# Kernel optimization log

Hardware: AMD Instinct MI355X
Metric: run time of the kernel (lower is better)

## Reference

```python
import jax, jax.numpy as jnp
import numpy as np

K = 3        # kernel_size
STRIDE = 1
PAD = 1
DIL = 1


def setup_inputs() -> dict:
    key = jax.random.key(0)
    k1, k2, k3 = jax.random.split(key, 3)
    B, C, H, W = 8, 256, 64, 64
    O = 256
    x = jax.random.normal(k1, (B, C, H, W), jnp.float32)
    # offset conv: Conv2d(C, 2*K*K, K, stride, pad) with bias
    w_off = jax.random.normal(k2, (2 * K * K, C, K, K), jnp.float32) * 0.01
    b_off = jnp.zeros((2 * K * K,), jnp.float32)
    # DeformConv weight (mmcv DeformConv has no bias)
    w_dcn = jax.random.normal(k3, (O, C, K, K), jnp.float32) * (1.0 / np.sqrt(C * K * K))
    return {"x": x, "w_off": w_off, "b_off": b_off, "w_dcn": w_dcn}


def _conv(x, w):
    return jax.lax.conv_general_dilated(
        x, w, window_strides=(STRIDE, STRIDE),
        padding=[(PAD, PAD), (PAD, PAD)], rhs_dilation=(DIL, DIL),
        dimension_numbers=("NCHW", "OIHW", "NCHW"))


def _bilinear(img_flat, y, x, H, W):
    # img_flat: [C, H*W]; y, x: [KK, Ho, Wo] float sampling coords
    y0 = jnp.floor(y)
    x0 = jnp.floor(x)
    out = jnp.zeros((img_flat.shape[0],) + y.shape, img_flat.dtype)
    for dy in (0.0, 1.0):
        for dx in (0.0, 1.0):
            yi = y0 + dy
            xi = x0 + dx
            wgt = (1.0 - jnp.abs(y - yi)) * (1.0 - jnp.abs(x - xi))
            valid = (yi >= 0) & (yi < H) & (xi >= 0) & (xi < W)
            yc = jnp.clip(yi, 0, H - 1).astype(jnp.int32)
            xc = jnp.clip(xi, 0, W - 1).astype(jnp.int32)
            idx = yc * W + xc                       # [KK,Ho,Wo]
            g = jnp.take(img_flat, idx.reshape(-1), axis=1)
            g = g.reshape((img_flat.shape[0],) + y.shape)  # [C,KK,Ho,Wo]
            out = out + g * (wgt * valid)[None]
    return out


def reference(x, w_off, b_off, w_dcn):
    B, C, H, W = x.shape
    O = w_dcn.shape[0]
    # 1) predict offsets: [B, 2*K*K, Ho, Wo], channel order (ky,kx) pairs per tap
    offset = _conv(x, w_off) + b_off[None, :, None, None]
    Ho, Wo = offset.shape[2], offset.shape[3]
    off = offset.reshape(B, K * K, 2, Ho, Wo)
    off_y = off[:, :, 0]   # [B,KK,Ho,Wo]
    off_x = off[:, :, 1]
    # 2) base sampling grid for a standard conv
    ky, kx = jnp.meshgrid(jnp.arange(K), jnp.arange(K), indexing="ij")
    ky = ky.reshape(-1).astype(x.dtype)   # [KK]
    kx = kx.reshape(-1).astype(x.dtype)
    hy = (jnp.arange(Ho) * STRIDE - PAD).astype(x.dtype)
    wx = (jnp.arange(Wo) * STRIDE - PAD).astype(x.dtype)
    base_y = hy[None, :, None] + (ky * DIL)[:, None, None]  # [KK,Ho,1]
    base_x = wx[None, None, :] + (kx * DIL)[:, None, None]  # [KK,1,Wo]
    sy = off_y + base_y[None]   # [B,KK,Ho,Wo]
    sx = off_x + base_x[None]
    # 3) bilinear gather: sampled patches [B,C,KK,Ho,Wo]
    img_flat = x.reshape(B, C, H * W)
    sampled = jax.vmap(lambda im, yy, xx: _bilinear(im, yy, xx, H, W))(img_flat, sy, sx)
    # 4) weighted sum over (C, kernel taps)
    out = jnp.einsum("bckhw,ock->bohw", sampled, w_dcn.reshape(O, C, K * K))
    return out
```

## Files before the change

### kernel.cpp

```cpp
#include <hip/hip_runtime.h>
#include <hip/hip_bf16.h>


#define HW 64
#define CCH 256
#define OCH 256
#define BB 8
#define KDIM 2304

typedef __attribute__((ext_vector_type(8))) short bf16x8;
typedef __attribute__((ext_vector_type(8))) unsigned short u16x8;
typedef __attribute__((ext_vector_type(4))) float f32x4;
typedef __attribute__((ext_vector_type(2))) float f32x2;
typedef __attribute__((ext_vector_type(4))) unsigned short u16x4;
typedef __attribute__((ext_vector_type(4))) unsigned int u32x4;

static __device__ inline unsigned short f2bf(float f) {
  unsigned u = __builtin_bit_cast(unsigned, f);
  u += 0x7FFFu + ((u >> 16) & 1u);
  return (unsigned short)(u >> 16);
}
static __device__ inline float bf2f(unsigned short s) {
  return __builtin_bit_cast(float, (unsigned)s << 16);
}
static __device__ inline unsigned cvt_pk_bf16(float lo, float hi) {
  unsigned r;
  asm("v_cvt_pk_bf16_f32 %0, %1, %2" : "=v"(r) : "v"(lo), "v"(hi));
  return r;
}

#define GLL16(gsrc, ldst)                                                      \
  __builtin_amdgcn_global_load_lds(                                           \
      (const __attribute__((address_space(1))) void*)(gsrc),                  \
      (__attribute__((address_space(3))) void*)(ldst), 16, 0, 0)

static __device__ inline int xcd_swz256(int bid) {
  return (bid & 7) * 32 + (bid >> 3);
}

__global__ __launch_bounds__(256) void prep(const float* __restrict__ w_dcn,
                                            const float* __restrict__ w_off,
                                            unsigned short* __restrict__ W2,
                                            unsigned short* __restrict__ Wop,
                                            unsigned short* __restrict__ zp) {
  int i = blockIdx.x * 256 + threadIdx.x;
  if (i < 9 * 256 * 256) {
    int o = i / KDIM;
    int r = i - o * KDIM;
    int kk = r >> 8, c = r & 255;
    W2[i] = f2bf(w_dcn[((o << 8) + c) * 9 + kk]);
  }
  if (i < 32 * KDIM) {
    int n = i / KDIM;
    int r = i - n * KDIM;
    int kk = r >> 8, c = r & 255;
    Wop[i] = (n < 18) ? f2bf(w_off[((n << 8) + c) * 9 + kk]) : (unsigned short)0;
  }
  if (i < 512) zp[i] = 0;
}

__global__ __launch_bounds__(256) void xpose(const float* __restrict__ x,
                                             unsigned short* __restrict__ xTbf) {
  __shared__ float t[64][65];
  const int tid = threadIdx.x;
  const int bid = blockIdx.x;
  const int ct = bid & 3;
  const int pt = (bid >> 2) & 63;
  const int b = bid >> 8;
#pragma unroll
  for (int i = 0; i < 16; ++i) {
    int cl = i * 4 + (tid >> 6);
    int p = tid & 63;
    t[cl][p] = x[(((b << 8) + ct * 64 + cl) << 12) + pt * 64 + p];
  }
  __syncthreads();
#pragma unroll
  for (int i = 0; i < 4; ++i) {
    int pl = i * 16 + (tid >> 4);
    int c4 = (tid & 15) * 4;
    u16x4 v;
    v[0] = f2bf(t[c4][pl]);
    v[1] = f2bf(t[c4 + 1][pl]);
    v[2] = f2bf(t[c4 + 2][pl]);
    v[3] = f2bf(t[c4 + 3][pl]);
    *(u16x4*)(xTbf + (((size_t)((b << 12) + pt * 64 + pl)) << 8) + ct * 64 + c4) = v;
  }
}

__global__ __launch_bounds__(256) void offset_gemm(
    const unsigned short* __restrict__ xTbf, const unsigned short* __restrict__ Wop,
    const unsigned short* __restrict__ zp, const float* __restrict__ b_off,
    float* __restrict__ off_buf) {
  __shared__ short ldsA[2][128 * 32];
  __shared__ short ldsB[2][32 * 32];
  const int tid = threadIdx.x;
  const int lane = tid & 63;
  const int wid = __builtin_amdgcn_readfirstlane(tid >> 6);
  const int m0 = xcd_swz256(blockIdx.x) * 128;
  const int b = m0 >> 12;
  const unsigned short* xb = xTbf + ((size_t)b << 20);

  int hA[2], wA[2], scA[2];
#pragma unroll
  for (int g = 0; g < 2; ++g) {
    int r = wid * 32 + g * 16 + (lane >> 2);
    int pos = (m0 & 4095) + r;
    hA[g] = pos >> 6;
    wA[g] = pos & 63;
    scA[g] = ((lane & 3) ^ ((r >> 1) & 3)) * 8;
  }
  const int rB = wid * 16 + (lane >> 2);
  const unsigned short* srcB =
      Wop + (size_t)rB * KDIM + ((lane & 3) ^ ((rB >> 1) & 3)) * 8;

  const int l15 = lane & 15, l4 = lane >> 4;
  int offA[2], offB[2];
#pragma unroll
  for (int f = 0; f < 2; ++f) {
    int rA = wid * 32 + f * 16 + l15;
    offA[f] = rA * 32 + ((l4 ^ ((rA >> 1) & 3)) << 3);
    int rb = f * 16 + l15;
    offB[f] = rb * 32 + ((l4 ^ ((rb >> 1) & 3)) << 3);
  }

  const f32x4 z = {0.f, 0.f, 0.f, 0.f};
  f32x4 acc[2][2];
#pragma unroll
  for (int i = 0; i < 2; ++i)
#pragma unroll
    for (int j = 0; j < 2; ++j) acc[i][j] = z;

  auto stage = [&](int buf, int t) {
    const int kk = t >> 3;
    const int c0 = (t & 7) * 32;
    const int dy = kk / 3 - 1, dx = kk - (kk / 3) * 3 - 1;
#pragma unroll
    for (int g = 0; g < 2; ++g) {
      const int y = hA[g] + dy, xx = wA[g] + dx;
      const bool valid = ((unsigned)y < 64u) && ((unsigned)xx < 64u);
      const unsigned short* src =
          valid ? xb + ((((y << 6) + xx) << 8) + c0 + scA[g]) : zp + scA[g];
      GLL16(src, &ldsA[buf][((wid * 2 + g) * 64 + lane) * 8]);
    }
    if (wid < 2) GLL16(srcB + t * 32, &ldsB[buf][(wid * 64 + lane) * 8]);
  };

  stage(0, 0);
  __syncthreads();

  for (int t = 0; t < 72; ++t) {
    const int buf = t & 1;
    if (t < 71) stage(buf ^ 1, t + 1);
    bf16x8 af[2], bfr[2];
#pragma unroll
    for (int f = 0; f < 2; ++f) af[f] = *(const bf16x8*)&ldsA[buf][offA[f]];
#pragma unroll
    for (int f = 0; f < 2; ++f) bfr[f] = *(const bf16x8*)&ldsB[buf][offB[f]];
#pragma unroll
    for (int i = 0; i < 2; ++i)
#pragma unroll
      for (int j = 0; j < 2; ++j)
        acc[i][j] = __builtin_amdgcn_mfma_f32_16x16x32_bf16(af[i], bfr[j],
                                                            acc[i][j], 0, 0, 0);
    __syncthreads();
  }

#pragma unroll
  for (int j = 0; j < 2; ++j) {
    const int col = j * 16 + l15;
    if (col < 18) {
      const float bias = b_off[col];
#pragma unroll
      for (int i = 0; i < 2; ++i)
#pragma unroll
        for (int r = 0; r < 4; ++r) {
          const int m = m0 + wid * 32 + i * 16 + l4 * 4 + r;
          off_buf[(size_t)m * 18 + col] = acc[i][j][r] + bias;
        }
    }
  }
}

__global__ __launch_bounds__(512, 2) void dcn_fused(
    const unsigned short* __restrict__ xTbf, const float* __restrict__ off_buf,
    const unsigned short* __restrict__ W2, float* __restrict__ out) {
  __shared__ f32x2 slyx[128][9];
  __shared__ u16x4 spos[128][9];
  __shared__ short ldsA[2][128 * 64];
  __shared__ short ldsB[2][256 * 64];

  const int tid = threadIdx.x;
  const int lane = tid & 63;
  const int wid = __builtin_amdgcn_readfirstlane(tid >> 6);
  const int m0 = xcd_swz256(blockIdx.x) * 128;
  const int b = m0 >> 12;
  const unsigned short* xb = xTbf + ((size_t)b << 20);

  for (int idx = tid; idx < 128 * 9; idx += 512) {
    const int r = idx / 9, k = idx - (idx / 9) * 9;
    const int ky = k / 3, kx = k - ky * 3;
    const int pos = (m0 & 4095) + r;
    const int h = pos >> 6, w = pos & 63;
    const float offy = off_buf[(size_t)(m0 + r) * 18 + 2 * k];
    const float offx = off_buf[(size_t)(m0 + r) * 18 + 2 * k + 1];
    const float sy = offy + (float)(h - 1 + ky);
    const float sx = offx + (float)(w - 1 + kx);
    const float y0f = floorf(sy), x0f = floorf(sx);
    const int y0 = (int)y0f, x0 = (int)x0f;
    const int y1 = y0 + 1, x1 = x0 + 1;
    const unsigned vy0 = ((unsigned)y0 < 64u), vy1 = ((unsigned)y1 < 64u);
    const unsigned vx0 = ((unsigned)x0 < 64u), vx1 = ((unsigned)x1 < 64u);
    const int y0c = min(max(y0, 0), HW - 1), y1c = min(max(y1, 0), HW - 1);
    const int x0c = min(max(x0, 0), HW - 1), x1c = min(max(x1, 0), HW - 1);
    f32x2 lyx;
    lyx[0] = sy - y0f;
    lyx[1] = sx - x0f;
    u16x4 pp;
    pp[0] = (unsigned short)(((y0c << 6) + x0c) | ((vy0 & vx0) << 15));
    pp[1] = (unsigned short)(((y0c << 6) + x1c) | ((vy0 & vx1) << 15));
    pp[2] = (unsigned short)(((y1c << 6) + x0c) | ((vy1 & vx0) << 15));
    pp[3] = (unsigned short)(((y1c << 6) + x1c) | ((vy1 & vx1) << 15));
    slyx[r][k] = lyx;
    spos[r][k] = pp;
  }

  const int r = tid >> 2, q = tid & 3;
  const int dstA0 = r * 64 + (((2 * q) ^ (r & 7)) << 3);
  const int dstA1 = r * 64 + (((2 * q + 1) ^ (r & 7)) << 3);

  const unsigned short* srcBp[4];
  int dstB[4];
#pragma unroll
  for (int g = 0; g < 4; ++g) {
    const int idx = g * 512 + tid;
    const int row = idx >> 3, c = idx & 7;
    srcBp[g] = W2 + (size_t)row * KDIM + ((c ^ (row & 7)) << 3);
    dstB[g] = idx * 8;
  }

  const int l15 = lane & 15, l4 = lane >> 4;
  const int wm = wid & 1, wn = wid >> 1;
  int offA[4][2], offB[4][2];
#pragma unroll
  for (int f = 0; f < 4; ++f) {
    const int rA = wm * 64 + f * 16 + l15;
    const int rB = wn * 64 + f * 16 + l15;
#pragma unroll
    for (int h = 0; h < 2; ++h) {
      offA[f][h] = rA * 64 + (((h * 4 + l4) ^ (rA & 7)) << 3);
      offB[f][h] = rB * 64 + (((h * 4 + l4) ^ (rB & 7)) << 3);
    }
  }

  const f32x4 z = {0.f, 0.f, 0.f, 0.f};
  f32x4 acc[4][4];
#pragma unroll
  for (int i = 0; i < 4; ++i)
#pragma unroll
    for (int j = 0; j < 4; ++j) acc[i][j] = z;

  __syncthreads();

  f32x4 wv;
  int av[4];
  auto load_params = [&](int tap) {
    const f32x2 lyx = slyx[r][tap];
    const u16x4 pp = spos[r][tap];
    const float ly = lyx[0], lx = lyx[1];
#pragma unroll
    for (int e = 0; e < 4; ++e) av[e] = (int)(pp[e] & 0x0FFFu) << 8;
    wv[0] = (1.f - ly) * (1.f - lx) * (float)(pp[0] >> 15);
    wv[1] = (1.f - ly) * lx * (float)(pp[1] >> 15);
    wv[2] = ly * (1.f - lx) * (float)(pp[2] >> 15);
    wv[3] = ly * lx * (float)(pp[3] >> 15);
  };

  u16x8 gc0[2], gc1[2], gc2[2], gc3[2];
  f32x4 gw;

  auto issue_gathers = [&](int t) {
    const int cb = ((t & 3) << 6) + q * 16;
#pragma unroll
    for (int h = 0; h < 2; ++h) {
      gc0[h] = *(const u16x8*)(xb + av[0] + cb + h * 8);
      gc1[h] = *(const u16x8*)(xb + av[1] + cb + h * 8);
      gc2[h] = *(const u16x8*)(xb + av[2] + cb + h * 8);
      gc3[h] = *(const u16x8*)(xb + av[3] + cb + h * 8);
    }
    gw = wv;
  };

  auto lerp_store = [&](int buf) {
    short* base = ldsA[buf];
#pragma unroll
    for (int h = 0; h < 2; ++h) {
      u32x4 wds;
#pragma unroll
      for (int e = 0; e < 4; ++e) {
        const float f0 = gw[0] * bf2f(gc0[h][2 * e]) + gw[1] * bf2f(gc1[h][2 * e]) +
                         gw[2] * bf2f(gc2[h][2 * e]) + gw[3] * bf2f(gc3[h][2 * e]);
        const float f1 = gw[0] * bf2f(gc0[h][2 * e + 1]) +
                         gw[1] * bf2f(gc1[h][2 * e + 1]) +
                         gw[2] * bf2f(gc2[h][2 * e + 1]) +
                         gw[3] * bf2f(gc3[h][2 * e + 1]);
        wds[e] = cvt_pk_bf16(f0, f1);
      }
      *(u32x4*)&base[h == 0 ? dstA0 : dstA1] = wds;
    }
  };

  load_params(0);
  issue_gathers(0);
  lerp_store(0);
#pragma unroll
  for (int g = 0; g < 4; ++g) GLL16(srcBp[g], &ldsB[0][dstB[g]]);
  __syncthreads();

  for (int t = 0; t < 36; ++t) {
    const int buf = t & 1;
    if (t < 35) {
      const int tn = t + 1;
#pragma unroll
      for (int g = 0; g < 4; ++g) GLL16(srcBp[g] + tn * 64, &ldsB[buf ^ 1][dstB[g]]);
      if ((tn & 3) == 0) load_params(tn >> 2);
      issue_gathers(tn);
    }
#pragma unroll
    for (int h = 0; h < 2; ++h) {
      bf16x8 af[4], bfr[4];
#pragma unroll
      for (int f = 0; f < 4; ++f) {
        af[f] = *(const bf16x8*)&ldsA[buf][offA[f][h]];
        bfr[f] = *(const bf16x8*)&ldsB[buf][offB[f][h]];
      }
#pragma unroll
      for (int i = 0; i < 4; ++i)
#pragma unroll
        for (int j = 0; j < 4; ++j)
          acc[i][j] = __builtin_amdgcn_mfma_f32_16x16x32_bf16(af[i], bfr[j],
                                                              acc[i][j], 0, 0, 0);
    }
    if (t < 35) lerp_store(buf ^ 1);
    __syncthreads();
  }

#pragma unroll
  for (int i = 0; i < 4; ++i) {
    const int m = m0 + wm * 64 + i * 16 + l4 * 4;
    const int bb = m >> 12;
    const int pos = m & 4095;
#pragma unroll
    for (int j = 0; j < 4; ++j) {
      const int o = wn * 64 + j * 16 + l15;
      *(f32x4*)(out + (((size_t)bb * OCH + o) << 12) + pos) = acc[i][j];
    }
  }
}

extern "C" void kernel_launch(void* const* d_in, const int* in_sizes, int n_in,
                              void* d_out, int out_size, void* d_ws,
                              size_t ws_size, hipStream_t stream) {
  const float* x = (const float*)d_in[0];
  const float* w_off = (const float*)d_in[1];
  const float* b_off = (const float*)d_in[2];
  const float* w_dcn = (const float*)d_in[3];
  float* out = (float*)d_out;

  char* ws = (char*)d_ws;
  float* off_buf = (float*)(ws);
  unsigned short* Wop = (unsigned short*)(ws + 2359296);
  unsigned short* zp = (unsigned short*)(ws + 2506752);
  unsigned short* W2 = (unsigned short*)(ws + 2507776);
  unsigned short* xTbf = (unsigned short*)(ws + 3687424);

  prep<<<2304, 256, 0, stream>>>(w_dcn, w_off, W2, Wop, zp);
  xpose<<<2048, 256, 0, stream>>>(x, xTbf);
  offset_gemm<<<256, 256, 0, stream>>>(xTbf, Wop, zp, b_off, off_buf);
  dcn_fused<<<256, 512, 0, stream>>>(xTbf, off_buf, W2, out);
}
```

Baseline: 124.4 us.

## Warp-specialize fused DCN kernel into producer gather waves and MFMA consumer waves

Splits the 8 waves of the fused deformable-conv GEMM into 4 producer waves and 4 consumer waves. The producers do the bilinear gathers, the lerp into LDS and the async weight loads. The consumers only read LDS and issue MFMAs, each over a 64x128 tile, with raised priority. The K-step shrinks from 64 to 32, which halves LDS buffers and doubles the iteration count, and gathers are prefetched two steps ahead with manual waitcnt and barrier handshakes. The aim is to overlap the latency-bound gather and lerp work with tensor-core compute. The cost is more barriers, higher register pressure in consumers (128 accumulator floats), and fragile hand-written vmcnt counts.

```diff
diff --git a/kernel.cpp b/kernel.cpp
--- a/kernel.cpp
+++ b/kernel.cpp
@@ -186,8 +186,8 @@
     const unsigned short* __restrict__ W2, float* __restrict__ out) {
   __shared__ f32x2 slyx[128][9];
   __shared__ u16x4 spos[128][9];
-  __shared__ short ldsA[2][128 * 64];
-  __shared__ short ldsB[2][256 * 64];
+  __shared__ short ldsA[2][128 * 32];
+  __shared__ short ldsB[2][256 * 32];
 
   const int tid = threadIdx.x;
   const int lane = tid & 63;
@@ -223,136 +223,176 @@
     slyx[r][k] = lyx;
     spos[r][k] = pp;
   }
-
-  const int r = tid >> 2, q = tid & 3;
-  const int dstA0 = r * 64 + (((2 * q) ^ (r & 7)) << 3);
-  const int dstA1 = r * 64 + (((2 * q + 1) ^ (r & 7)) << 3);
-
-  const unsigned short* srcBp[4];
-  int dstB[4];
-#pragma unroll
-  for (int g = 0; g < 4; ++g) {
-    const int idx = g * 512 + tid;
-    const int row = idx >> 3, c = idx & 7;
-    srcBp[g] = W2 + (size_t)row * KDIM + ((c ^ (row & 7)) << 3);
-    dstB[g] = idx * 8;
-  }
-
-  const int l15 = lane & 15, l4 = lane >> 4;
-  const int wm = wid & 1, wn = wid >> 1;
-  int offA[4][2], offB[4][2];
-#pragma unroll
-  for (int f = 0; f < 4; ++f) {
-    const int rA = wm * 64 + f * 16 + l15;
-    const int rB = wn * 64 + f * 16 + l15;
-#pragma unroll
-    for (int h = 0; h < 2; ++h) {
-      offA[f][h] = rA * 64 + (((h * 4 + l4) ^ (rA & 7)) << 3);
-      offB[f][h] = rB * 64 + (((h * 4 + l4) ^ (rB & 7)) << 3);
-    }
-  }
-
-  const f32x4 z = {0.f, 0.f, 0.f, 0.f};
-  f32x4 acc[4][4];
-#pragma unroll
-  for (int i = 0; i < 4; ++i)
-#pragma unroll
-    for (int j = 0; j < 4; ++j) acc[i][j] = z;
-
   __syncthreads();
 
-  f32x4 wv;
-  int av[4];
-  auto load_params = [&](int tap) {
-    const f32x2 lyx = slyx[r][tap];
-    const u16x4 pp = spos[r][tap];
-    const float ly = lyx[0], lx = lyx[1];
-#pragma unroll
-    for (int e = 0; e < 4; ++e) av[e] = (int)(pp[e] & 0x0FFFu) << 8;
-    wv[0] = (1.f - ly) * (1.f - lx) * (float)(pp[0] >> 15);
-    wv[1] = (1.f - ly) * lx * (float)(pp[1] >> 15);
-    wv[2] = ly * (1.f - lx) * (float)(pp[2] >> 15);
-    wv[3] = ly * lx * (float)(pp[3] >> 15);
-  };
-
-  u16x8 gc0[2], gc1[2], gc2[2], gc3[2];
-  f32x4 gw;
-
-  auto issue_gathers = [&](int t) {
-    const int cb = ((t & 3) << 6) + q * 16;
-#pragma unroll
-    for (int h = 0; h < 2; ++h) {
-      gc0[h] = *(const u16x8*)(xb + av[0] + cb + h * 8);
-      gc1[h] = *(const u16x8*)(xb + av[1] + cb + h * 8);
-      gc2[h] = *(const u16x8*)(xb + av[2] + cb + h * 8);
-      gc3[h] = *(const u16x8*)(xb + av[3] + cb + h * 8);
-    }
-    gw = wv;
-  };
-
-  auto lerp_store = [&](int buf) {
-    short* base = ldsA[buf];
-#pragma unroll
-    for (int h = 0; h < 2; ++h) {
-      u32x4 wds;
-#pragma unroll
-      for (int e = 0; e < 4; ++e) {
-        const float f0 = gw[0] * bf2f(gc0[h][2 * e]) + gw[1] * bf2f(gc1[h][2 * e]) +
-                         gw[2] * bf2f(gc2[h][2 * e]) + gw[3] * bf2f(gc3[h][2 * e]);
-        const float f1 = gw[0] * bf2f(gc0[h][2 * e + 1]) +
-                         gw[1] * bf2f(gc1[h][2 * e + 1]) +
-                         gw[2] * bf2f(gc2[h][2 * e + 1]) +
-                         gw[3] * bf2f(gc3[h][2 * e + 1]);
-        wds[e] = cvt_pk_bf16(f0, f1);
+  if (wid < 4) {
+    const int ptid = tid;
+    const int r = ptid >> 1;
+    const int g2 = ptid & 1;
+    const int g2h = g2 * 16;
+    const int dstA0 = r * 32 + (((2 * g2) ^ ((r >> 1) & 3)) << 3);
+    const int dstA1 = r * 32 + (((2 * g2 + 1) ^ ((r >> 1) & 3)) << 3);
+    const unsigned short* srcBp[4];
+    int dstB[4];
+#pragma unroll
+    for (int g = 0; g < 4; ++g) {
+      const int idx = g * 256 + ptid;
+      const int row = idx >> 2, c = idx & 3;
+      srcBp[g] = W2 + (size_t)row * KDIM + ((c ^ ((row >> 1) & 3)) << 3);
+      dstB[g] = idx * 8;
+    }
+
+    f32x4 wv;
+    int av[4];
+    auto load_params = [&](int tap) {
+      const f32x2 lyx = slyx[r][tap];
+      const u16x4 pp = spos[r][tap];
+      const float ly = lyx[0], lx = lyx[1];
+#pragma unroll
+      for (int e = 0; e < 4; ++e) av[e] = (int)(pp[e] & 0x0FFFu) << 8;
+      wv[0] = (1.f - ly) * (1.f - lx) * (float)(pp[0] >> 15);
+      wv[1] = (1.f - ly) * lx * (float)(pp[1] >> 15);
+      wv[2] = ly * (1.f - lx) * (float)(pp[2] >> 15);
+      wv[3] = ly * lx * (float)(pp[3] >> 15);
+    };
+
+    auto lerp_store = [&](int buf, const u16x8 (&gc)[4][2], const f32x4& gw) {
+#pragma unroll
+      for (int h = 0; h < 2; ++h) {
+        u32x4 wds;
+#pragma unroll
+        for (int e = 0; e < 4; ++e) {
+          const float f0 =
+              gw[0] * bf2f(gc[0][h][2 * e]) + gw[1] * bf2f(gc[1][h][2 * e]) +
+              gw[2] * bf2f(gc[2][h][2 * e]) + gw[3] * bf2f(gc[3][h][2 * e]);
+          const float f1 = gw[0] * bf2f(gc[0][h][2 * e + 1]) +
+                           gw[1] * bf2f(gc[1][h][2 * e + 1]) +
+                           gw[2] * bf2f(gc[2][h][2 * e + 1]) +
+                           gw[3] * bf2f(gc[3][h][2 * e + 1]);
+          wds[e] = cvt_pk_bf16(f0, f1);
+        }
+        *(u32x4*)&ldsA[buf][h == 0 ? dstA0 : dstA1] = wds;
       }
-      *(u32x4*)&base[h == 0 ? dstA0 : dstA1] = wds;
-    }
-  };
-
-  load_params(0);
-  issue_gathers(0);
-  lerp_store(0);
-#pragma unroll
-  for (int g = 0; g < 4; ++g) GLL16(srcBp[g], &ldsB[0][dstB[g]]);
-  __syncthreads();
-
-  for (int t = 0; t < 36; ++t) {
-    const int buf = t & 1;
-    if (t < 35) {
-      const int tn = t + 1;
-#pragma unroll
-      for (int g = 0; g < 4; ++g) GLL16(srcBp[g] + tn * 64, &ldsB[buf ^ 1][dstB[g]]);
-      if ((tn & 3) == 0) load_params(tn >> 2);
-      issue_gathers(tn);
-    }
-#pragma unroll
-    for (int h = 0; h < 2; ++h) {
-      bf16x8 af[4], bfr[4];
-#pragma unroll
-      for (int f = 0; f < 4; ++f) {
-        af[f] = *(const bf16x8*)&ldsA[buf][offA[f][h]];
-        bfr[f] = *(const bf16x8*)&ldsB[buf][offB[f][h]];
+    };
+
+    u16x8 gA[4][2], gB[4][2];
+    f32x4 wA, wB;
+
+    load_params(0);
+    {
+#pragma unroll
+      for (int c = 0; c < 4; ++c) {
+        gA[c][0] = *(const u16x8*)(xb + av[c] + g2h);
+        gA[c][1] = *(const u16x8*)(xb + av[c] + g2h + 8);
       }
+      wA = wv;
+    }
+#pragma unroll
+    for (int g = 0; g < 4; ++g) GLL16(srcBp[g], &ldsB[0][dstB[g]]);
+    __builtin_amdgcn_sched_barrier(0);
+    lerp_store(0, gA, wA);
+    {
+#pragma unroll
+      for (int c = 0; c < 4; ++c) {
+        gA[c][0] = *(const u16x8*)(xb + av[c] + 32 + g2h);
+        gA[c][1] = *(const u16x8*)(xb + av[c] + 32 + g2h + 8);
+      }
+      wA = wv;
+    }
+    asm volatile("s_waitcnt vmcnt(8) lgkmcnt(0)" ::: "memory");
+    __builtin_amdgcn_s_barrier();
+
+#define PSTEP(T, IN, INW, OUT, OUTW)                                           \
+  {                                                                            \
+    const int tn = (T) + 1;                                                    \
+    _Pragma("unroll") for (int g = 0; g < 4; ++g)                              \
+        GLL16(srcBp[g] + tn * 32, &ldsB[tn & 1][dstB[g]]);                     \
+    __builtin_amdgcn_sched_barrier(0);                                         \
+    {                                                                          \
+      const int tg = (T) + 2;                                                  \
+      if ((tg & 7) == 0) load_params(tg >> 3);                                 \
+      const int cb = ((tg & 7) << 5) + g2h;                                    \
+      _Pragma("unroll") for (int c = 0; c < 4; ++c) {                          \
+        OUT[c][0] = *(const u16x8*)(xb + av[c] + cb);                          \
+        OUT[c][1] = *(const u16x8*)(xb + av[c] + cb + 8);                      \
+      }                                                                        \
+      OUTW = wv;                                                               \
+    }                                                                          \
+    lerp_store(tn & 1, IN, INW);                                               \
+    asm volatile("s_waitcnt vmcnt(8) lgkmcnt(0)" ::: "memory");                \
+    __builtin_amdgcn_s_barrier();                                              \
+  }
+
+    for (int it = 0; it < 35; ++it) {
+      const int t0 = it * 2;
+      PSTEP(t0, gA, wA, gB, wB)
+      PSTEP(t0 + 1, gB, wB, gA, wA)
+    }
+#undef PSTEP
+    {
+#pragma unroll
+      for (int g = 0; g < 4; ++g) GLL16(srcBp[g] + 71 * 32, &ldsB[1][dstB[g]]);
+      __builtin_amdgcn_sched_barrier(0);
+      lerp_store(1, gA, wA);
+      asm volatile("s_waitcnt vmcnt(0) lgkmcnt(0)" ::: "memory");
+      __builtin_amdgcn_s_barrier();
+    }
+  } else {
+    const int wc = wid - 4;
+    const int wm = wc & 1, wn = wc >> 1;
+    const int l15 = lane & 15, l4 = lane >> 4;
+    int offA[4], offB[8];
+#pragma unroll
+    for (int f = 0; f < 4; ++f) {
+      const int rA = wm * 64 + f * 16 + l15;
+      offA[f] = rA * 32 + ((l4 ^ ((rA >> 1) & 3)) << 3);
+    }
+#pragma unroll
+    for (int j = 0; j < 8; ++j) {
+      const int rB = wn * 128 + j * 16 + l15;
+      offB[j] = rB * 32 + ((l4 ^ ((rB >> 1) & 3)) << 3);
+    }
+
+    const f32x4 z = {0.f, 0.f, 0.f, 0.f};
+    f32x4 acc[4][8];
+#pragma unroll
+    for (int i = 0; i < 4; ++i)
+#pragma unroll
+      for (int j = 0; j < 8; ++j) acc[i][j] = z;
+
+    __builtin_amdgcn_s_barrier();
+
+    for (int t = 0; t < 72; ++t) {
+      const int buf = t & 1;
+      bf16x8 af[4], bfr[8];
+#pragma unroll
+      for (int f = 0; f < 4; ++f) af[f] = *(const bf16x8*)&ldsA[buf][offA[f]];
+#pragma unroll
+      for (int j = 0; j < 8; ++j) bfr[j] = *(const bf16x8*)&ldsB[buf][offB[j]];
+      __builtin_amdgcn_s_setprio(1);
 #pragma unroll
       for (int i = 0; i < 4; ++i)
 #pragma unroll
-        for (int j = 0; j < 4; ++j)
+        for (int j = 0; j < 8; ++j)
           acc[i][j] = __builtin_amdgcn_mfma_f32_16x16x32_bf16(af[i], bfr[j],
                                                               acc[i][j], 0, 0, 0);
-    }
-    if (t < 35) lerp_store(buf ^ 1);
-    __syncthreads();
-  }
-
-#pragma unroll
-  for (int i = 0; i < 4; ++i) {
-    const int m = m0 + wm * 64 + i * 16 + l4 * 4;
-    const int bb = m >> 12;
-    const int pos = m & 4095;
-#pragma unroll
-    for (int j = 0; j < 4; ++j) {
-      const int o = wn * 64 + j * 16 + l15;
-      *(f32x4*)(out + (((size_t)bb * OCH + o) << 12) + pos) = acc[i][j];
+      __builtin_amdgcn_s_setprio(0);
+      if (t < 71) {
+        asm volatile("s_waitcnt lgkmcnt(0)" ::: "memory");
+        __builtin_amdgcn_s_barrier();
+      }
+    }
+
+#pragma unroll
+    for (int i = 0; i < 4; ++i) {
+      const int m = m0 + wm * 64 + i * 16 + l4 * 4;
+      const int bb = m >> 12;
+      const int pos = m & 4095;
+#pragma unroll
+      for (int j = 0; j < 8; ++j) {
+        const int o = wn * 128 + j * 16 + l15;
+        *(f32x4*)(out + (((size_t)bb * OCH + o) << 12) + pos) = acc[i][j];
+      }
     }
   }
 }
```

After: 128.0 us. 1.03x slower.

## Stage spatial window of input in LDS per channel chunk for deformable gather

Applied to the files above, without the earlier changes.

Changes the bf16 transposed input layout to channel-chunked blocks of 32 channels. The DCN kernel loops channel chunk outer and tap inner. For each chunk it stages a 12-row spatial window of the input into LDS, and the bilinear gathers read from it when the sample falls inside the window, otherwise from global memory. The K-step shrinks to 32, and the MFMA issue gets raised priority. The goal is to replace scattered global gathers with LDS reads. The cost is more barriers, a stall whenever the window is reloaded, and more LDS use, which may lower occupancy.

```diff
diff --git a/kernel.cpp b/kernel.cpp
--- a/kernel.cpp
+++ b/kernel.cpp
@@ -78,12 +78,15 @@
   for (int i = 0; i < 4; ++i) {
     int pl = i * 16 + (tid >> 4);
     int c4 = (tid & 15) * 4;
+    int c = ct * 64 + c4;
+    int pos = pt * 64 + pl;
     u16x4 v;
     v[0] = f2bf(t[c4][pl]);
     v[1] = f2bf(t[c4 + 1][pl]);
     v[2] = f2bf(t[c4 + 2][pl]);
     v[3] = f2bf(t[c4 + 3][pl]);
-    *(u16x4*)(xTbf + (((size_t)((b << 12) + pt * 64 + pl)) << 8) + ct * 64 + c4) = v;
+    *(u16x4*)(xTbf + ((size_t)b << 20) + (c >> 5) * 131072 + pos * 32 +
+              (c & 31)) = v;
   }
 }
 
@@ -132,14 +135,15 @@
 
   auto stage = [&](int buf, int t) {
     const int kk = t >> 3;
-    const int c0 = (t & 7) * 32;
+    const int cc = t & 7;
     const int dy = kk / 3 - 1, dx = kk - (kk / 3) * 3 - 1;
 #pragma unroll
     for (int g = 0; g < 2; ++g) {
       const int y = hA[g] + dy, xx = wA[g] + dx;
       const bool valid = ((unsigned)y < 64u) && ((unsigned)xx < 64u);
       const unsigned short* src =
-          valid ? xb + ((((y << 6) + xx) << 8) + c0 + scA[g]) : zp + scA[g];
+          valid ? xb + cc * 131072 + ((y << 6) + xx) * 32 + scA[g]
+                : zp + scA[g];
       GLL16(src, &ldsA[buf][((wid * 2 + g) * 64 + lane) * 8]);
     }
     if (wid < 2) GLL16(srcB + t * 32, &ldsB[buf][(wid * 64 + lane) * 8]);
@@ -186,8 +190,9 @@
     const unsigned short* __restrict__ W2, float* __restrict__ out) {
   __shared__ f32x2 slyx[128][9];
   __shared__ u16x4 spos[128][9];
-  __shared__ short ldsA[2][128 * 64];
-  __shared__ short ldsB[2][256 * 64];
+  __shared__ short win[12 * 64 * 32];
+  __shared__ short ldsA[2][128 * 32];
+  __shared__ short ldsB[2][256 * 32];
 
   const int tid = threadIdx.x;
   const int lane = tid & 63;
@@ -195,7 +200,23 @@
   const int m0 = xcd_swz256(blockIdx.x) * 128;
   const int b = m0 >> 12;
   const unsigned short* xb = xTbf + ((size_t)b << 20);
-
+  const int h0 = (m0 & 4095) >> 6;
+  const int ys = max(0, h0 - 5);
+
+  auto stage_window = [&](int cc) {
+    const unsigned short* xbc = xb + cc * 131072;
+#pragma unroll
+    for (int g = 0; g < 6; ++g) {
+      const int o = g * 8192 + tid * 16;
+      const int rel = o >> 12;
+      const int xw = (o >> 6) & 63;
+      const int cs = (o & 63) >> 1;
+      const int ysrc = min(63, ys + rel);
+      GLL16(xbc + ((ysrc << 6) + xw) * 32 + cs, &win[o >> 1]);
+    }
+  };
+
+  stage_window(0);
   for (int idx = tid; idx < 128 * 9; idx += 512) {
     const int r = idx / 9, k = idx - (idx / 9) * 9;
     const int ky = k / 3, kx = k - ky * 3;
@@ -212,11 +233,13 @@
     const unsigned vx0 = ((unsigned)x0 < 64u), vx1 = ((unsigned)x1 < 64u);
     const int y0c = min(max(y0, 0), HW - 1), y1c = min(max(y1, 0), HW - 1);
     const int x0c = min(max(x0, 0), HW - 1), x1c = min(max(x1, 0), HW - 1);
+    const unsigned inwin = (y0c >= ys) & (y1c <= ys + 11);
     f32x2 lyx;
     lyx[0] = sy - y0f;
     lyx[1] = sx - x0f;
     u16x4 pp;
-    pp[0] = (unsigned short)(((y0c << 6) + x0c) | ((vy0 & vx0) << 15));
+    pp[0] = (unsigned short)(((y0c << 6) + x0c) | (inwin << 14) |
+                             ((vy0 & vx0) << 15));
     pp[1] = (unsigned short)(((y0c << 6) + x1c) | ((vy0 & vx1) << 15));
     pp[2] = (unsigned short)(((y1c << 6) + x0c) | ((vy1 & vx0) << 15));
     pp[3] = (unsigned short)(((y1c << 6) + x1c) | ((vy1 & vx1) << 15));
@@ -225,31 +248,27 @@
   }
 
   const int r = tid >> 2, q = tid & 3;
-  const int dstA0 = r * 64 + (((2 * q) ^ (r & 7)) << 3);
-  const int dstA1 = r * 64 + (((2 * q + 1) ^ (r & 7)) << 3);
-
-  const unsigned short* srcBp[4];
-  int dstB[4];
-#pragma unroll
-  for (int g = 0; g < 4; ++g) {
+  const int q8 = q * 8;
+  const int dstA = r * 32 + ((q ^ ((r >> 1) & 3)) << 3);
+  const unsigned short* srcBp[2];
+  int dstB[2];
+#pragma unroll
+  for (int g = 0; g < 2; ++g) {
     const int idx = g * 512 + tid;
-    const int row = idx >> 3, c = idx & 7;
-    srcBp[g] = W2 + (size_t)row * KDIM + ((c ^ (row & 7)) << 3);
+    const int row = idx >> 2, c = idx & 3;
+    srcBp[g] = W2 + (size_t)row * KDIM + ((c ^ ((row >> 1) & 3)) << 3);
     dstB[g] = idx * 8;
   }
 
   const int l15 = lane & 15, l4 = lane >> 4;
   const int wm = wid & 1, wn = wid >> 1;
-  int offA[4][2], offB[4][2];
+  int offA[4], offB[4];
 #pragma unroll
   for (int f = 0; f < 4; ++f) {
     const int rA = wm * 64 + f * 16 + l15;
+    offA[f] = rA * 32 + ((l4 ^ ((rA >> 1) & 3)) << 3);
     const int rB = wn * 64 + f * 16 + l15;
-#pragma unroll
-    for (int h = 0; h < 2; ++h) {
-      offA[f][h] = rA * 64 + (((h * 4 + l4) ^ (rA & 7)) << 3);
-      offB[f][h] = rB * 64 + (((h * 4 + l4) ^ (rB & 7)) << 3);
-    }
+    offB[f] = rB * 32 + ((l4 ^ ((rB >> 1) & 3)) << 3);
   }
 
   const f32x4 z = {0.f, 0.f, 0.f, 0.f};
@@ -259,89 +278,85 @@
 #pragma unroll
     for (int j = 0; j < 4; ++j) acc[i][j] = z;
 
-  __syncthreads();
-
-  f32x4 wv;
-  int av[4];
-  auto load_params = [&](int tap) {
+  auto produce = [&](int buf, int tap, int cc) {
     const f32x2 lyx = slyx[r][tap];
     const u16x4 pp = spos[r][tap];
     const float ly = lyx[0], lx = lyx[1];
-#pragma unroll
-    for (int e = 0; e < 4; ++e) av[e] = (int)(pp[e] & 0x0FFFu) << 8;
-    wv[0] = (1.f - ly) * (1.f - lx) * (float)(pp[0] >> 15);
-    wv[1] = (1.f - ly) * lx * (float)(pp[1] >> 15);
-    wv[2] = ly * (1.f - lx) * (float)(pp[2] >> 15);
-    wv[3] = ly * lx * (float)(pp[3] >> 15);
+    const float w0 = (1.f - ly) * (1.f - lx) * (float)(pp[0] >> 15);
+    const float w1 = (1.f - ly) * lx * (float)(pp[1] >> 15);
+    const float w2 = ly * (1.f - lx) * (float)(pp[2] >> 15);
+    const float w3 = ly * lx * (float)(pp[3] >> 15);
+    int po[4];
+#pragma unroll
+    for (int e = 0; e < 4; ++e) po[e] = pp[e] & 0x0FFF;
+    u16x8 c[4];
+    if (__builtin_expect((pp[0] >> 14) & 1, 1)) {
+#pragma unroll
+      for (int e = 0; e < 4; ++e)
+        c[e] = *(const u16x8*)&win[((po[e] >> 6) - ys) * 2048 +
+                                   (po[e] & 63) * 32 + q8];
+    } else {
+      const unsigned short* xbc = xb + cc * 131072;
+#pragma unroll
+      for (int e = 0; e < 4; ++e)
+        c[e] = *(const u16x8*)(xbc + po[e] * 32 + q8);
+    }
+    u32x4 wds;
+#pragma unroll
+    for (int e = 0; e < 4; ++e) {
+      const float f0 = w0 * bf2f(c[0][2 * e]) + w1 * bf2f(c[1][2 * e]) +
+                       w2 * bf2f(c[2][2 * e]) + w3 * bf2f(c[3][2 * e]);
+      const float f1 = w0 * bf2f(c[0][2 * e + 1]) + w1 * bf2f(c[1][2 * e + 1]) +
+                       w2 * bf2f(c[2][2 * e + 1]) + w3 * bf2f(c[3][2 * e + 1]);
+      wds[e] = cvt_pk_bf16(f0, f1);
+    }
+    *(u32x4*)&ldsA[buf][dstA] = wds;
   };
 
-  u16x8 gc0[2], gc1[2], gc2[2], gc3[2];
-  f32x4 gw;
-
-  auto issue_gathers = [&](int t) {
-    const int cb = ((t & 3) << 6) + q * 16;
-#pragma unroll
-    for (int h = 0; h < 2; ++h) {
-      gc0[h] = *(const u16x8*)(xb + av[0] + cb + h * 8);
-      gc1[h] = *(const u16x8*)(xb + av[1] + cb + h * 8);
-      gc2[h] = *(const u16x8*)(xb + av[2] + cb + h * 8);
-      gc3[h] = *(const u16x8*)(xb + av[3] + cb + h * 8);
-    }
-    gw = wv;
-  };
-
-  auto lerp_store = [&](int buf) {
-    short* base = ldsA[buf];
-#pragma unroll
-    for (int h = 0; h < 2; ++h) {
-      u32x4 wds;
-#pragma unroll
-      for (int e = 0; e < 4; ++e) {
-        const float f0 = gw[0] * bf2f(gc0[h][2 * e]) + gw[1] * bf2f(gc1[h][2 * e]) +
-                         gw[2] * bf2f(gc2[h][2 * e]) + gw[3] * bf2f(gc3[h][2 * e]);
-        const float f1 = gw[0] * bf2f(gc0[h][2 * e + 1]) +
-                         gw[1] * bf2f(gc1[h][2 * e + 1]) +
-                         gw[2] * bf2f(gc2[h][2 * e + 1]) +
-                         gw[3] * bf2f(gc3[h][2 * e + 1]);
-        wds[e] = cvt_pk_bf16(f0, f1);
+  GLL16(srcBp[0], &ldsB[0][dstB[0]]);
+  GLL16(srcBp[1], &ldsB[0][dstB[1]]);
+  asm volatile("s_waitcnt vmcnt(0) lgkmcnt(0)" ::: "memory");
+  __builtin_amdgcn_s_barrier();
+  produce(0, 0, 0);
+  __syncthreads();
+
+  int t = 0;
+  for (int cc = 0; cc < 8; ++cc) {
+    for (int tap = 0; tap < 9; ++tap, ++t) {
+      const int buf = t & 1;
+      const bool last = (t == 71);
+      if (!last) {
+        const int tapn = (tap == 8) ? 0 : tap + 1;
+        const int ccn = (tap == 8) ? cc + 1 : cc;
+        const int koff = tapn * 256 + ccn * 32;
+        GLL16(srcBp[0] + koff, &ldsB[buf ^ 1][dstB[0]]);
+        GLL16(srcBp[1] + koff, &ldsB[buf ^ 1][dstB[1]]);
+        if (tap != 8) produce(buf ^ 1, tapn, cc);
       }
-      *(u32x4*)&base[h == 0 ? dstA0 : dstA1] = wds;
-    }
-  };
-
-  load_params(0);
-  issue_gathers(0);
-  lerp_store(0);
-#pragma unroll
-  for (int g = 0; g < 4; ++g) GLL16(srcBp[g], &ldsB[0][dstB[g]]);
-  __syncthreads();
-
-  for (int t = 0; t < 36; ++t) {
-    const int buf = t & 1;
-    if (t < 35) {
-      const int tn = t + 1;
-#pragma unroll
-      for (int g = 0; g < 4; ++g) GLL16(srcBp[g] + tn * 64, &ldsB[buf ^ 1][dstB[g]]);
-      if ((tn & 3) == 0) load_params(tn >> 2);
-      issue_gathers(tn);
-    }
-#pragma unroll
-    for (int h = 0; h < 2; ++h) {
       bf16x8 af[4], bfr[4];
 #pragma unroll
       for (int f = 0; f < 4; ++f) {
-        af[f] = *(const bf16x8*)&ldsA[buf][offA[f][h]];
-        bfr[f] = *(const bf16x8*)&ldsB[buf][offB[f][h]];
+        af[f] = *(const bf16x8*)&ldsA[buf][offA[f]];
+        bfr[f] = *(const bf16x8*)&ldsB[buf][offB[f]];
       }
+      __builtin_amdgcn_s_setprio(1);
 #pragma unroll
       for (int i = 0; i < 4; ++i)
 #pragma unroll
         for (int j = 0; j < 4; ++j)
           acc[i][j] = __builtin_amdgcn_mfma_f32_16x16x32_bf16(af[i], bfr[j],
                                                               acc[i][j], 0, 0, 0);
-    }
-    if (t < 35) lerp_store(buf ^ 1);
-    __syncthreads();
+      __builtin_amdgcn_s_setprio(0);
+      if (!last && tap == 8) {
+        stage_window(cc + 1);
+        asm volatile("s_waitcnt vmcnt(0) lgkmcnt(0)" ::: "memory");
+        __builtin_amdgcn_s_barrier();
+        produce(buf ^ 1, 0, cc + 1);
+        __syncthreads();
+      } else {
+        __syncthreads();
+      }
+    }
   }
 
 #pragma unroll
```

New measurement: 135.3 us. 8.8% more time.
